# Optimization experiments

Hardware: AMD Instinct MI355X
Metric: run time of the kernel (lower is better)

The kernel has to match this reference:

```python
import jax, jax.numpy as jnp
import numpy as np

KB = 0.0019872041      # Boltzmann constant, kcal/(mol*K)
TEMP = 300.0
ALPHA = 10.0
BW = 0.15              # Gaussian KDE bandwidth
PAIR_I = jnp.array([0, 0, 0, 1, 1, 2])
PAIR_J = jnp.array([1, 2, 3, 2, 3, 3])

B, N_ATOMS = 512, 1024
G, L, K, D = 256, 8, 128, 6


def setup_inputs() -> dict:
    key = jax.random.key(0)
    k1, k2, k3, k4, k5, k6 = jax.random.split(key, 6)
    positions = jax.random.normal(k1, (B, N_ATOMS, 3), dtype=jnp.float32) * 2.0
    # KDE training samples live in 6-dim distance space (positive, few Angstroms)
    kde_samples = jax.random.uniform(k2, (G, L, K, D), dtype=jnp.float32) * 5.0
    weight = jax.random.uniform(k3, (G, L), dtype=jnp.float32)
    offset = jax.random.normal(k4, (G, L), dtype=jnp.float32)
    atom_idxs = jax.random.randint(k5, (G, L, 4), 0, N_ATOMS)
    group_sizes = jax.random.randint(k6, (G,), 0, L)  # clamped to >=1 in reference
    return {"positions": positions, "kde_samples": kde_samples, "weight": weight,
            "offset": offset, "atom_idxs": atom_idxs, "group_sizes": group_sizes}


def reference(positions, kde_samples, weight, offset, atom_idxs, group_sizes):
    Gn, Ln, Kn, Dn = kde_samples.shape
    # Gather the 4 vertices of every loss: [B, G, L, 4, 3]
    vp = positions[:, atom_idxs]
    # 6 pairwise distances per loss: [B, G, L, 6]
    diff = vp[..., PAIR_I, :] - vp[..., PAIR_J, :]
    dists = jnp.sqrt(jnp.sum(diff * diff, axis=-1) + 1e-12)
    # Gaussian KDE log-density over the K training samples, expanded squared
    x2 = jnp.sum(dists * dists, axis=-1)          # [B,G,L]
    mu2 = jnp.sum(kde_samples * kde_samples, -1)  # [G,L,K]
    xmu = jnp.einsum('bgld,glkd->bglk', dists, kde_samples)
    sq = x2[..., None] + mu2[None] - 2.0 * xmu    # [B,G,L,K]
    log_norm = jnp.log(jnp.float32(Kn)) + 0.5 * Dn * jnp.log(2.0 * jnp.pi * BW * BW)
    logP = jax.nn.logsumexp(-sq / (2.0 * BW * BW), axis=-1) - log_norm  # [B,G,L]
    energy = -KB * TEMP * logP
    scaled = energy * weight + offset             # [B,G,L]
    # Ragged group reduction: min over the valid losses of each group
    sizes = jnp.maximum(group_sizes, 1)
    mask = jnp.arange(Ln)[None, :] < sizes[:, None]        # [G,L]
    group_min = jnp.min(jnp.where(mask, scaled, jnp.inf), axis=-1)  # [B,G]
    # soft-min across groups
    return -jax.nn.logsumexp(-ALPHA * group_min, axis=-1) / ALPHA   # [B]
```

## Files before the change

kernel.cpp:

```cpp
#include <hip/hip_runtime.h>

#define NB 512
#define NATOMS 1024
#define NG 256
#define NL 8
#define NK 128

#define KBT 0.59616123f
#define ALPHA_C 10.0f
#define LN2 0.6931471805599453f
#define LOG2E 1.4426950408889634f
#define INV2BW2 22.222221f
#define SCALE2 (INV2BW2 * LOG2E)
#define LOG_NORM (-1.0170649f)

#define WL_CAP 2048

typedef _Float16 f16x8 __attribute__((ext_vector_type(8)));
typedef float f32x16 __attribute__((ext_vector_type(16)));

__device__ __forceinline__ float fexp2(float x) { return __builtin_amdgcn_exp2f(x); }
__device__ __forceinline__ float flog2(float x) { return __builtin_amdgcn_logf(x); }

__device__ __forceinline__ float wred_min(float v) {
#pragma unroll
  for (int m = 32; m >= 1; m >>= 1) v = fminf(v, __shfl_xor(v, m, 64));
  return v;
}
__device__ __forceinline__ float wred_sum(float v) {
#pragma unroll
  for (int m = 32; m >= 1; m >>= 1) v += __shfl_xor(v, m, 64);
  return v;
}

__global__ __launch_bounds__(256) void prep_wl(
    const int* __restrict__ gsizes, int* __restrict__ wl) {
  const int t = threadIdx.x;
  const int lane = t & 63, wid = t >> 6;
  int gs = gsizes[t];
  int nl = gs < 1 ? 1 : (gs > NL ? NL : gs);
  int x = nl;
#pragma unroll
  for (int m = 1; m < 64; m <<= 1) {
    int y = __shfl_up(x, m, 64);
    if (lane >= m) x += y;
  }
  __shared__ int wsum[4];
  if (lane == 63) wsum[wid] = x;
  __syncthreads();
  int off = 0;
  for (int i = 0; i < wid; ++i) off += wsum[i];
  int inc = off + x, exc = inc - nl;
  for (int j = 0; j < nl; ++j) wl[exc + j] = (t << 3) | j;
  if (t == 255) wl[WL_CAP] = inc;
}

__global__ __launch_bounds__(256) void stage1_kernel(
    const float* __restrict__ positions, const float* __restrict__ kde,
    const float* __restrict__ weight, const float* __restrict__ offs,
    const int* __restrict__ atom_idxs, const int* __restrict__ wl,
    float* __restrict__ scaled_out) {
  const int count = wl[WL_CAP];
  const int w = blockIdx.x >> 2;
  if (w >= count) return;
  const int gl = wl[w];

  const int t = threadIdx.x;
  const int lane = t & 63;
  const int col = lane & 31, h = lane >> 5;
  const int b = ((blockIdx.x & 3) << 7) + ((t >> 6) << 5) + col;

  __shared__ f16x8 tabL[8][64];

  const int4 idx = *reinterpret_cast<const int4*>(atom_idxs + (gl << 2));
  const int ids[4] = {idx.x, idx.y, idx.z, idx.w};
  const float* pb = positions + (size_t)b * NATOMS * 3;
  float ax[4], ay[4], az[4];
#pragma unroll
  for (int j = 0; j < 4; ++j) {
    const float3 p = *reinterpret_cast<const float3*>(pb + ids[j] * 3);
    ax[j] = p.x; ay[j] = p.y; az[j] = p.z;
  }

  if (t < NK) {
    const float* mp = kde + ((size_t)gl * NK + t) * 6;
    float mu2 = 0.0f;
    _Float16 ah[6], al[6];
#pragma unroll
    for (int q = 0; q < 6; ++q) {
      float mv = mp[q];
      mu2 += mv * mv;
      float a = (2.0f * SCALE2) * mv;
      _Float16 hh = (_Float16)a;
      ah[q] = hh;
      al[q] = (_Float16)(a - (float)hh);
    }
    float z = -SCALE2 * mu2;
    _Float16 z1 = (_Float16)z;
    _Float16 z2 = (_Float16)(z - (float)z1);
    const _Float16 Z = (_Float16)0.0f;
    const int kt = t >> 5, m = t & 31;
    tabL[kt * 2 + 0][m]      = (f16x8){ah[0],ah[1],ah[2],ah[3],ah[4],ah[5],al[0],al[1]};
    tabL[kt * 2 + 0][m + 32] = (f16x8){al[2],al[3],al[4],al[5],ah[0],ah[1],ah[2],ah[3]};
    tabL[kt * 2 + 1][m]      = (f16x8){ah[4],ah[5],al[0],al[1],al[2],al[3],al[4],al[5]};
    tabL[kt * 2 + 1][m + 32] = (f16x8){z1,  z2,  Z,   Z,   Z,   Z,   Z,   Z   };
  }

  const int PI_[6] = {0, 0, 0, 1, 1, 2};
  const int PJ_[6] = {1, 2, 3, 2, 3, 3};
  float d[6]; float x2 = 0.0f;
#pragma unroll
  for (int q = 0; q < 6; ++q) {
    float dx = ax[PI_[q]] - ax[PJ_[q]];
    float dy = ay[PI_[q]] - ay[PJ_[q]];
    float dz = az[PI_[q]] - az[PJ_[q]];
    float dd = dx * dx + dy * dy + dz * dz + 1e-12f;
    d[q] = sqrtf(dd);
    x2 += d[q] * d[q];
  }
  const float c2 = -x2 * SCALE2;

  _Float16 xh[6], xl[6];
#pragma unroll
  for (int q = 0; q < 6; ++q) {
    _Float16 hh = (_Float16)d[q];
    xh[q] = hh;
    xl[q] = (_Float16)(d[q] - (float)hh);
  }
  const _Float16 ONE = (_Float16)1.0f, Z = (_Float16)0.0f;
  f16x8 Bf0 = (h == 0)
    ? (f16x8){xh[0],xh[1],xh[2],xh[3],xh[4],xh[5],xh[0],xh[1]}
    : (f16x8){xh[2],xh[3],xh[4],xh[5],xl[0],xl[1],xl[2],xl[3]};
  f16x8 Bf1 = (h == 0)
    ? (f16x8){xl[4],xl[5],xl[0],xl[1],xl[2],xl[3],xl[4],xl[5]}
    : (f16x8){ONE,  ONE,  Z,   Z,   Z,   Z,   Z,   Z   };

  __syncthreads();

  const f32x16 zz = {0.0f};
  f32x16 acc[4];
#pragma unroll
  for (int kt = 0; kt < 4; ++kt) {
    f16x8 A0 = tabL[kt * 2 + 0][lane];
    f16x8 A1 = tabL[kt * 2 + 1][lane];
    acc[kt] = __builtin_amdgcn_mfma_f32_32x32x16_f16(
        A1, Bf1, __builtin_amdgcn_mfma_f32_32x32x16_f16(A0, Bf0, zz, 0, 0, 0),
        0, 0, 0);
  }

  float mkt[4];
#pragma unroll
  for (int kt = 0; kt < 4; ++kt) {
    float m0 = fmaxf(fmaxf(acc[kt][0], acc[kt][1]), fmaxf(acc[kt][2], acc[kt][3]));
    float m1 = fmaxf(fmaxf(acc[kt][4], acc[kt][5]), fmaxf(acc[kt][6], acc[kt][7]));
    float m2 = fmaxf(fmaxf(acc[kt][8], acc[kt][9]), fmaxf(acc[kt][10], acc[kt][11]));
    float m3 = fmaxf(fmaxf(acc[kt][12], acc[kt][13]), fmaxf(acc[kt][14], acc[kt][15]));
    mkt[kt] = fmaxf(fmaxf(m0, m1), fmaxf(m2, m3));
  }
  float mx = fmaxf(fmaxf(mkt[0], mkt[1]), fmaxf(mkt[2], mkt[3]));
  mx = fmaxf(mx, __shfl_xor(mx, 32, 64));

  float s0 = 0.0f, s1 = 0.0f, s2 = 0.0f, s3 = 0.0f;
#pragma unroll
  for (int kt = 0; kt < 4; ++kt) {
    s0 += fexp2(acc[kt][0] - mx)  + fexp2(acc[kt][1] - mx)
        + fexp2(acc[kt][2] - mx)  + fexp2(acc[kt][3] - mx);
    s1 += fexp2(acc[kt][4] - mx)  + fexp2(acc[kt][5] - mx)
        + fexp2(acc[kt][6] - mx)  + fexp2(acc[kt][7] - mx);
    s2 += fexp2(acc[kt][8] - mx)  + fexp2(acc[kt][9] - mx)
        + fexp2(acc[kt][10] - mx) + fexp2(acc[kt][11] - mx);
    s3 += fexp2(acc[kt][12] - mx) + fexp2(acc[kt][13] - mx)
        + fexp2(acc[kt][14] - mx) + fexp2(acc[kt][15] - mx);
  }
  float s = (s0 + s1) + (s2 + s3);
  s += __shfl_xor(s, 32, 64);

  if (h == 0) {
    float lse2 = c2 + mx + flog2(s);
    float logP = lse2 * LN2 - LOG_NORM;
    float sc = -KBT * logP * weight[gl] + offs[gl];
    scaled_out[(size_t)gl * NB + b] = sc;
  }
}

__global__ __launch_bounds__(256) void stage2_kernel(
    const float* __restrict__ scaled_in, const int* __restrict__ gsizes,
    float* __restrict__ out) {
  const int b = blockIdx.x;
  const int t = threadIdx.x;
  const int lane = t & 63;
  const int wid = t >> 6;
  int gs = gsizes[t];
  int nl = gs < 1 ? 1 : (gs > NL ? NL : gs);
  float v = 1e30f;
  for (int l = 0; l < nl; ++l)
    v = fminf(v, scaled_in[(size_t)((t << 3) + l) * NB + b]);

  __shared__ float sm[4], ss[4];
  float m = wred_min(v);
  if (lane == 0) sm[wid] = m;
  __syncthreads();
  float M = fminf(fminf(sm[0], sm[1]), fminf(sm[2], sm[3]));
  float e = fexp2(-ALPHA_C * LOG2E * (v - M));
  float s = wred_sum(e);
  if (lane == 0) ss[wid] = s;
  __syncthreads();
  if (t == 0) {
    float S = ss[0] + ss[1] + ss[2] + ss[3];
    out[b] = M - flog2(S) * LN2 / ALPHA_C;
  }
}

extern "C" void kernel_launch(void* const* d_in, const int* in_sizes, int n_in,
                              void* d_out, int out_size, void* d_ws, size_t ws_size,
                              hipStream_t stream) {
  const float* positions = (const float*)d_in[0];
  const float* kde       = (const float*)d_in[1];
  const float* weight    = (const float*)d_in[2];
  const float* offs      = (const float*)d_in[3];
  const int*   atom_idxs = (const int*)d_in[4];
  const int*   gsizes    = (const int*)d_in[5];
  float* out = (float*)d_out;

  float* scaled = (float*)d_ws;
  int* wl = (int*)((char*)d_ws + (4 << 20));

  prep_wl<<<dim3(1), dim3(256), 0, stream>>>(gsizes, wl);
  stage1_kernel<<<dim3(WL_CAP * 4), dim3(256), 0, stream>>>(
      positions, kde, weight, offs, atom_idxs, wl, scaled);
  stage2_kernel<<<dim3(NB), dim3(256), 0, stream>>>(scaled, gsizes, out);
}
```

Measured before the change: 38.71 us.

## Build KDE MFMA operands in registers and use online two-pass logsumexp

Every wave now loads the KDE samples and builds its f16 hi/lo A-operand fragments in registers, replacing the shared-memory table and the block barrier. The logsumexp runs as an online (running max and rescaled sum) reduction over two passes of two MFMA tiles, so fewer accumulators stay live at once. This removes LDS traffic and the __syncthreads, which should improve occupancy. The cost is that the same KDE rows are loaded and converted redundantly in each of the four waves, plus extra exp2 rescaling work.

```diff
diff --git a/kernel.cpp b/kernel.cpp
--- a/kernel.cpp
+++ b/kernel.cpp
@@ -70,8 +70,6 @@
   const int col = lane & 31, h = lane >> 5;
   const int b = ((blockIdx.x & 3) << 7) + ((t >> 6) << 5) + col;
 
-  __shared__ f16x8 tabL[8][64];
-
   const int4 idx = *reinterpret_cast<const int4*>(atom_idxs + (gl << 2));
   const int ids[4] = {idx.x, idx.y, idx.z, idx.w};
   const float* pb = positions + (size_t)b * NATOMS * 3;
@@ -82,28 +80,14 @@
     ax[j] = p.x; ay[j] = p.y; az[j] = p.z;
   }
 
-  if (t < NK) {
-    const float* mp = kde + ((size_t)gl * NK + t) * 6;
-    float mu2 = 0.0f;
-    _Float16 ah[6], al[6];
-#pragma unroll
-    for (int q = 0; q < 6; ++q) {
-      float mv = mp[q];
-      mu2 += mv * mv;
-      float a = (2.0f * SCALE2) * mv;
-      _Float16 hh = (_Float16)a;
-      ah[q] = hh;
-      al[q] = (_Float16)(a - (float)hh);
-    }
-    float z = -SCALE2 * mu2;
-    _Float16 z1 = (_Float16)z;
-    _Float16 z2 = (_Float16)(z - (float)z1);
-    const _Float16 Z = (_Float16)0.0f;
-    const int kt = t >> 5, m = t & 31;
-    tabL[kt * 2 + 0][m]      = (f16x8){ah[0],ah[1],ah[2],ah[3],ah[4],ah[5],al[0],al[1]};
-    tabL[kt * 2 + 0][m + 32] = (f16x8){al[2],al[3],al[4],al[5],ah[0],ah[1],ah[2],ah[3]};
-    tabL[kt * 2 + 1][m]      = (f16x8){ah[4],ah[5],al[0],al[1],al[2],al[3],al[4],al[5]};
-    tabL[kt * 2 + 1][m + 32] = (f16x8){z1,  z2,  Z,   Z,   Z,   Z,   Z,   Z   };
+  float kr[4][6];
+#pragma unroll
+  for (int kt = 0; kt < 4; ++kt) {
+    const float2* rp = reinterpret_cast<const float2*>(
+        kde + ((size_t)gl * NK + kt * 32 + col) * 6);
+    float2 r0 = rp[0], r1 = rp[1], r2 = rp[2];
+    kr[kt][0] = r0.x; kr[kt][1] = r0.y; kr[kt][2] = r1.x;
+    kr[kt][3] = r1.y; kr[kt][4] = r2.x; kr[kt][5] = r2.y;
   }
 
   const int PI_[6] = {0, 0, 0, 1, 1, 2};
@@ -135,48 +119,67 @@
     ? (f16x8){xl[4],xl[5],xl[0],xl[1],xl[2],xl[3],xl[4],xl[5]}
     : (f16x8){ONE,  ONE,  Z,   Z,   Z,   Z,   Z,   Z   };
 
-  __syncthreads();
-
   const f32x16 zz = {0.0f};
-  f32x16 acc[4];
-#pragma unroll
-  for (int kt = 0; kt < 4; ++kt) {
-    f16x8 A0 = tabL[kt * 2 + 0][lane];
-    f16x8 A1 = tabL[kt * 2 + 1][lane];
-    acc[kt] = __builtin_amdgcn_mfma_f32_32x32x16_f16(
-        A1, Bf1, __builtin_amdgcn_mfma_f32_32x32x16_f16(A0, Bf0, zz, 0, 0, 0),
-        0, 0, 0);
-  }
-
-  float mkt[4];
-#pragma unroll
-  for (int kt = 0; kt < 4; ++kt) {
-    float m0 = fmaxf(fmaxf(acc[kt][0], acc[kt][1]), fmaxf(acc[kt][2], acc[kt][3]));
-    float m1 = fmaxf(fmaxf(acc[kt][4], acc[kt][5]), fmaxf(acc[kt][6], acc[kt][7]));
-    float m2 = fmaxf(fmaxf(acc[kt][8], acc[kt][9]), fmaxf(acc[kt][10], acc[kt][11]));
-    float m3 = fmaxf(fmaxf(acc[kt][12], acc[kt][13]), fmaxf(acc[kt][14], acc[kt][15]));
-    mkt[kt] = fmaxf(fmaxf(m0, m1), fmaxf(m2, m3));
-  }
-  float mx = fmaxf(fmaxf(mkt[0], mkt[1]), fmaxf(mkt[2], mkt[3]));
-  mx = fmaxf(mx, __shfl_xor(mx, 32, 64));
-
-  float s0 = 0.0f, s1 = 0.0f, s2 = 0.0f, s3 = 0.0f;
-#pragma unroll
-  for (int kt = 0; kt < 4; ++kt) {
-    s0 += fexp2(acc[kt][0] - mx)  + fexp2(acc[kt][1] - mx)
-        + fexp2(acc[kt][2] - mx)  + fexp2(acc[kt][3] - mx);
-    s1 += fexp2(acc[kt][4] - mx)  + fexp2(acc[kt][5] - mx)
-        + fexp2(acc[kt][6] - mx)  + fexp2(acc[kt][7] - mx);
-    s2 += fexp2(acc[kt][8] - mx)  + fexp2(acc[kt][9] - mx)
-        + fexp2(acc[kt][10] - mx) + fexp2(acc[kt][11] - mx);
-    s3 += fexp2(acc[kt][12] - mx) + fexp2(acc[kt][13] - mx)
-        + fexp2(acc[kt][14] - mx) + fexp2(acc[kt][15] - mx);
-  }
-  float s = (s0 + s1) + (s2 + s3);
-  s += __shfl_xor(s, 32, 64);
+  float mloc = -1e30f, sloc = 0.0f;
+#pragma unroll
+  for (int pass = 0; pass < 2; ++pass) {
+    f32x16 aa[2];
+#pragma unroll
+    for (int i = 0; i < 2; ++i) {
+      const int kt = pass * 2 + i;
+      float mu2 = 0.0f;
+      _Float16 ah[6], al[6];
+#pragma unroll
+      for (int q = 0; q < 6; ++q) {
+        float mv = kr[kt][q];
+        mu2 += mv * mv;
+        float a = (2.0f * SCALE2) * mv;
+        _Float16 hh = (_Float16)a;
+        ah[q] = hh;
+        al[q] = (_Float16)(a - (float)hh);
+      }
+      float z = -SCALE2 * mu2;
+      _Float16 z1 = (_Float16)z;
+      _Float16 z2 = (_Float16)(z - (float)z1);
+      f16x8 A0 = (h == 0)
+        ? (f16x8){ah[0],ah[1],ah[2],ah[3],ah[4],ah[5],al[0],al[1]}
+        : (f16x8){al[2],al[3],al[4],al[5],ah[0],ah[1],ah[2],ah[3]};
+      f16x8 A1 = (h == 0)
+        ? (f16x8){ah[4],ah[5],al[0],al[1],al[2],al[3],al[4],al[5]}
+        : (f16x8){z1,  z2,  Z,   Z,   Z,   Z,   Z,   Z   };
+      aa[i] = __builtin_amdgcn_mfma_f32_32x32x16_f16(
+          A1, Bf1, __builtin_amdgcn_mfma_f32_32x32x16_f16(A0, Bf0, zz, 0, 0, 0),
+          0, 0, 0);
+    }
+    float m0 = fmaxf(fmaxf(aa[0][0], aa[0][1]), fmaxf(aa[0][2], aa[0][3]));
+    float m1 = fmaxf(fmaxf(aa[0][4], aa[0][5]), fmaxf(aa[0][6], aa[0][7]));
+    float m2 = fmaxf(fmaxf(aa[0][8], aa[0][9]), fmaxf(aa[0][10], aa[0][11]));
+    float m3 = fmaxf(fmaxf(aa[0][12], aa[0][13]), fmaxf(aa[0][14], aa[0][15]));
+    float m4 = fmaxf(fmaxf(aa[1][0], aa[1][1]), fmaxf(aa[1][2], aa[1][3]));
+    float m5 = fmaxf(fmaxf(aa[1][4], aa[1][5]), fmaxf(aa[1][6], aa[1][7]));
+    float m6 = fmaxf(fmaxf(aa[1][8], aa[1][9]), fmaxf(aa[1][10], aa[1][11]));
+    float m7 = fmaxf(fmaxf(aa[1][12], aa[1][13]), fmaxf(aa[1][14], aa[1][15]));
+    float mp = fmaxf(fmaxf(fmaxf(m0, m1), fmaxf(m2, m3)),
+                     fmaxf(fmaxf(m4, m5), fmaxf(m6, m7)));
+    float s0 = 0.0f, s1 = 0.0f;
+#pragma unroll
+    for (int i = 0; i < 16; ++i) {
+      s0 += fexp2(aa[0][i] - mp);
+      s1 += fexp2(aa[1][i] - mp);
+    }
+    float sp = s0 + s1;
+    float nm = fmaxf(mloc, mp);
+    sloc = fmaf(sloc, fexp2(mloc - nm), sp * fexp2(mp - nm));
+    mloc = nm;
+  }
+
+  float mo = __shfl_xor(mloc, 32, 64);
+  float so = __shfl_xor(sloc, 32, 64);
+  float M = fmaxf(mloc, mo);
+  float S = sloc * fexp2(mloc - M) + so * fexp2(mo - M);
 
   if (h == 0) {
-    float lse2 = c2 + mx + flog2(s);
+    float lse2 = c2 + M + flog2(S);
     float logP = lse2 * LN2 - LOG_NORM;
     float sc = -KBT * logP * weight[gl] + offs[gl];
     scaled_out[(size_t)gl * NB + b] = sc;
```

Result: slower. 40.40 us (+4.4%).
